# Optimization experiments

Measured on AMD Instinct MI355X. Metric: run time of the kernel, lower is better.

The kernel has to match this reference:

```python
import jax, jax.numpy as jnp
import numpy as np

N_ROLES = 6
EPS = 1e-5

def _ln(x, scale, bias):
    m = jnp.mean(x, axis=-1, keepdims=True)
    v = jnp.var(x, axis=-1, keepdims=True)
    return (x - m) * jax.lax.rsqrt(v + EPS) * scale + bias

def setup_inputs() -> dict:
    key = jax.random.key(0)
    ks = jax.random.split(key, 20)
    T, B, D_OBS, H, A = 32, 1024, 256, 512, 32
    inp = {
        'rnn_states': jax.random.normal(ks[0], (B, H), jnp.float32),
        'obs': jax.random.normal(ks[1], (T, B, D_OBS), jnp.float32),
        'resets': jnp.zeros((T, B), jnp.float32),
        'available_actions': jnp.ones((T, B, A), jnp.float32),
        'role_ids': jax.random.randint(ks[2], (T, B), 0, N_ROLES, jnp.int32),
        # feature norm over obs_dim
        'fn_scale': jnp.ones((D_OBS,), jnp.float32),
        'fn_bias': jnp.zeros((D_OBS,), jnp.float32),
        # base MLP: obs_dim->512->512, each followed by LayerNorm
        'W0': jax.random.normal(ks[3], (D_OBS, H), jnp.float32) * 0.02,
        'b0': jnp.zeros((H,), jnp.float32),
        'ln0_scale': jnp.ones((H,), jnp.float32),
        'ln0_bias': jnp.zeros((H,), jnp.float32),
        'W1': jax.random.normal(ks[4], (H, H), jnp.float32) * 0.02,
        'b1': jnp.zeros((H,), jnp.float32),
        'ln1_scale': jnp.ones((H,), jnp.float32),
        'ln1_bias': jnp.zeros((H,), jnp.float32),
        # per-role routes: obs_dim->128->H (stacked over roles)
        'Wr0': jax.random.normal(ks[5], (N_ROLES, D_OBS, 128), jnp.float32) * 0.02,
        'br0': jnp.zeros((N_ROLES, 128), jnp.float32),
        'Wr1': jax.random.normal(ks[6], (N_ROLES, 128, H), jnp.float32) * 0.02,
        'br1': jnp.zeros((N_ROLES, H), jnp.float32),
        # per-role heads: H->64->32->action_dim (stacked over roles)
        'Wh0': jax.random.normal(ks[7], (N_ROLES, H, 64), jnp.float32) * 0.02,
        'bh0': jnp.zeros((N_ROLES, 64), jnp.float32),
        'Wh1': jax.random.normal(ks[8], (N_ROLES, 64, 32), jnp.float32) * 0.02,
        'bh1': jnp.zeros((N_ROLES, 32), jnp.float32),
        'Wh2': jax.random.normal(ks[9], (N_ROLES, 32, A), jnp.float32) * 0.02,
        'bh2': jnp.zeros((N_ROLES, A), jnp.float32),
    }
    return inp

def _gather_by_role(all_values, role_ids):
    # all_values: (K, T, B, F); role_ids: (T, B) -> (T, B, F)
    idx = role_ids[None, :, :, None].astype(jnp.int32)
    return jnp.take_along_axis(all_values, idx, axis=0)[0]

def reference(rnn_states, obs, resets, available_actions, role_ids,
              fn_scale, fn_bias, W0, b0, ln0_scale, ln0_bias,
              W1, b1, ln1_scale, ln1_bias,
              Wr0, br0, Wr1, br1,
              Wh0, bh0, Wh1, bh1, Wh2, bh2):
    # feature normalization on raw obs
    obs_n = _ln(obs, fn_scale, fn_bias)
    # shared base MLP (relu + LayerNorm after each Dense)
    e = _ln(jax.nn.relu(obs_n @ W0 + b0), ln0_scale, ln0_bias)
    e = _ln(jax.nn.relu(e @ W1 + b1), ln1_scale, ln1_bias)
    # per-role pre-GRU residual routes on (normalized) obs
    r = jax.nn.relu(jnp.einsum('tbi,kih->ktbh', obs_n, Wr0) + br0[:, None, None, :])
    r = jax.nn.relu(jnp.einsum('ktbh,kho->ktbo', r, Wr1) + br1[:, None, None, :])
    e = e + _gather_by_role(r, role_ids)
    # no recurrent policy configured: rnn_states pass through
    # per-role heads -> all logits (K, T, B, A)
    h = jax.nn.relu(jnp.einsum('tbh,khf->ktbf', e, Wh0) + bh0[:, None, None, :])
    h = jax.nn.relu(jnp.einsum('ktbf,kfg->ktbg', h, Wh1) + bh1[:, None, None, :])
    all_logits = jnp.einsum('ktbg,kga->ktba', h, Wh2) + bh2[:, None, None, :]
    logits = _gather_by_role(all_logits, role_ids)
    logits = jnp.where(available_actions > 0.5, logits, jnp.full_like(logits, -1e10))
    return rnn_states, logits
```

## Files before the change

kernel.cpp:

```cpp
#include <hip/hip_runtime.h>
#include <stdint.h>

typedef unsigned short u16;
typedef unsigned int u32;

using bf16x8 = __attribute__((ext_vector_type(8))) short;
using f32x4  = __attribute__((ext_vector_type(4))) float;

#define DEVINL __device__ __forceinline__

DEVINL float b2f(u16 u) { return __builtin_bit_cast(float, (u32)u << 16); }
DEVINL u16 f2b(float f) {
  u32 u = __builtin_bit_cast(u32, f);
  u += 0x7FFFu + ((u >> 16) & 1u);
  return (u16)(u >> 16);
}

DEVINL void tp_tile(const float* __restrict__ s, u16* __restrict__ d,
                    int R, int C, int bx, int by, int z)
{
  __shared__ u16 tile[32][33];
  const size_t mstride = (size_t)R * C;
  s += (size_t)z * mstride;
  d += (size_t)z * mstride;
  int r0 = bx * 32, c0 = by * 32;
  int tx = threadIdx.x & 31, ty = threadIdx.x >> 5;
#pragma unroll
  for (int i = 0; i < 32; i += 8)
    tile[ty + i][tx] = f2b(s[(size_t)(r0 + ty + i) * C + (c0 + tx)]);
  __syncthreads();
#pragma unroll
  for (int i = 0; i < 32; i += 8)
    d[(size_t)(c0 + ty + i) * R + (r0 + tx)] = tile[tx][ty + i];
}

__global__ __launch_bounds__(256) void transpose_all(
    const float* W0, const float* W1, const float* Wr0, const float* Wr1, const float* Wh0,
    u16* W0t, u16* W1t, u16* Wr0t, u16* Wr1t, u16* Wh0t)
{
  int b = blockIdx.x;
  if (b < 128)      {            tp_tile(W0, W0t, 256, 512, b % 8,  b / 8, 0); }
  else if (b < 384) { b -= 128;  tp_tile(W1, W1t, 512, 512, b % 16, b / 16, 0); }
  else if (b < 576) { b -= 384;  int t = b / 8;  tp_tile(Wr0, Wr0t, 256, 128, b % 8,  t % 4,  t / 4); }
  else if (b < 960) { b -= 576;  int t = b / 4;  tp_tile(Wr1, Wr1t, 128, 512, b % 4,  t % 16, t / 16); }
  else              { b -= 960;  int t = b / 16; tp_tile(Wh0, Wh0t, 512, 64,  b % 16, t % 2,  t / 2); }
}

__global__ __launch_bounds__(256) void ln_f32_256(
    const float* __restrict__ X, const float* __restrict__ sc,
    const float* __restrict__ bi, u16* __restrict__ Y, int nrows)
{
  constexpr int D = 256, PER = 4;
  int lane = threadIdx.x & 63;
  int row = blockIdx.x * 4 + (threadIdx.x >> 6);
  if (row >= nrows) return;
  const float* xr = X + (size_t)row * D + lane * PER;
  float x[PER] __attribute__((aligned(16)));
  *(float4*)x = *(const float4*)xr;
  float s = 0.f, s2 = 0.f;
#pragma unroll
  for (int p = 0; p < PER; ++p) { s += x[p]; s2 += x[p] * x[p]; }
#pragma unroll
  for (int o = 32; o > 0; o >>= 1) { s += __shfl_xor(s, o, 64); s2 += __shfl_xor(s2, o, 64); }
  float m = s * (1.f / D);
  float v = s2 * (1.f / D) - m * m;
  float inv = rsqrtf(v + 1e-5f);
  u16 yu[PER] __attribute__((aligned(8)));
#pragma unroll
  for (int p = 0; p < PER; ++p)
    yu[p] = f2b((x[p] - m) * inv * sc[lane * PER + p] + bi[lane * PER + p]);
  *(uint2*)(Y + (size_t)row * D + lane * PER) = *(uint2*)yu;
}

__global__ __launch_bounds__(256) void ln_bf16_512(
    const u16* __restrict__ X, const float* __restrict__ sc,
    const float* __restrict__ bi, u16* __restrict__ Y, int nrows)
{
  constexpr int D = 512, PER = 8;
  int lane = threadIdx.x & 63;
  int row = blockIdx.x * 4 + (threadIdx.x >> 6);
  if (row >= nrows) return;
  const u16* xr = X + (size_t)row * D + lane * PER;
  u16 xu[PER] __attribute__((aligned(16)));
  *(uint4*)xu = *(const uint4*)xr;
  float x[PER]; float s = 0.f, s2 = 0.f;
#pragma unroll
  for (int p = 0; p < PER; ++p) { x[p] = b2f(xu[p]); s += x[p]; s2 += x[p] * x[p]; }
#pragma unroll
  for (int o = 32; o > 0; o >>= 1) { s += __shfl_xor(s, o, 64); s2 += __shfl_xor(s2, o, 64); }
  float m = s * (1.f / D);
  float v = s2 * (1.f / D) - m * m;
  float inv = rsqrtf(v + 1e-5f);
  u16 yu[PER] __attribute__((aligned(16)));
#pragma unroll
  for (int p = 0; p < PER; ++p)
    yu[p] = f2b((x[p] - m) * inv * sc[lane * PER + p] + bi[lane * PER + p]);
  *(uint4*)(Y + (size_t)row * D + lane * PER) = *(uint4*)yu;
}

#define NROLE 6
__global__ __launch_bounds__(256) void role_count(
    const int* __restrict__ rid, int* __restrict__ blkCnt)
{
  __shared__ int h[NROLE];
  if (threadIdx.x < NROLE) h[threadIdx.x] = 0;
  __syncthreads();
  int i = blockIdx.x * 256 + threadIdx.x;
  atomicAdd(&h[rid[i]], 1);
  __syncthreads();
  if (threadIdx.x < NROLE) blkCnt[blockIdx.x * NROLE + threadIdx.x] = h[threadIdx.x];
}

__global__ __launch_bounds__(256) void role_scan(
    const int* __restrict__ blkCnt, int* __restrict__ blkBase,
    int* __restrict__ baseArr, int* __restrict__ cntArr)
{
  __shared__ int c[128 * NROLE];
  __shared__ int bb[128 * NROLE];
  __shared__ int sbase[NROLE], scnt[NROLE];
  for (int i = threadIdx.x; i < 128 * NROLE; i += 256) c[i] = blkCnt[i];
  __syncthreads();
  if (threadIdx.x < NROLE) {
    int k = threadIdx.x, run = 0;
    for (int b = 0; b < 128; ++b) { bb[b * NROLE + k] = run; run += c[b * NROLE + k]; }
    scnt[k] = run;
  }
  __syncthreads();
  if (threadIdx.x == 0) {
    int r = 0;
    for (int k = 0; k < NROLE; ++k) { sbase[k] = r; r += scnt[k]; }
  }
  __syncthreads();
  if (threadIdx.x < NROLE) { baseArr[threadIdx.x] = sbase[threadIdx.x]; cntArr[threadIdx.x] = scnt[threadIdx.x]; }
  for (int i = threadIdx.x; i < 128 * NROLE; i += 256)
    blkBase[i] = bb[i] + sbase[i % NROLE];
}

__global__ __launch_bounds__(256) void role_fill(
    const int* __restrict__ rid, const int* __restrict__ blkBase, int* __restrict__ bucket)
{
  __shared__ int h[NROLE];
  if (threadIdx.x < NROLE) h[threadIdx.x] = 0;
  __syncthreads();
  int i = blockIdx.x * 256 + threadIdx.x;
  int k = rid[i];
  int pos = atomicAdd(&h[k], 1);
  bucket[blkBase[blockIdx.x * NROLE + k] + pos] = i;
}

enum { GM_DENSE = 0, GM_GATHER = 1, GM_CONTIG = 2, GM_GATHER_ADD = 3 };

template <int BN, int MODE>
__global__ __launch_bounds__(512, 4) void gemm_bf16(
    const u16* __restrict__ A, const u16* __restrict__ Bt,
    const float* __restrict__ bias, u16* __restrict__ C,
    const u16* __restrict__ E,
    const int* __restrict__ bucket, const int* __restrict__ baseArr,
    const int* __restrict__ cntArr, int M, int N, int K, int ldc)
{
  constexpr int BM = 256, BK = 64;
  constexpr int NF = BN / 32;
  constexpr int BR = BN / 64;
  __shared__ __align__(16) u16 As[BM * BK];
  __shared__ __align__(16) u16 Bs[BN * BK];
  const int tid = threadIdx.x;
  const int role = blockIdx.z;
  const int rowBase = blockIdx.x * BM;
  int limit;
  if constexpr (MODE == GM_DENSE) limit = M; else limit = cntArr[role];
  if (rowBase >= limit) return;
  int roleBase = 0;
  if constexpr (MODE != GM_DENSE) roleBase = baseArr[role];
  const u16* BtK = Bt + (size_t)role * N * K + (size_t)blockIdx.y * BN * K;
  const float* biasK = bias + (size_t)role * N + (size_t)blockIdx.y * BN;

  const int lane = tid & 63;
  const int wave = tid >> 6;

  const int swcol = (((tid & 7) ^ ((tid >> 3) & 7)) * 8);

  u32 aOff[4];
#pragma unroll
  for (int r = 0; r < 4; ++r) {
    int arow = r * 64 + (tid >> 3);
    int i = rowBase + arow;
    if (i >= limit) i = rowBase;
    int grow;
    if constexpr (MODE == GM_DENSE)       grow = i;
    else if constexpr (MODE == GM_GATHER) grow = bucket[roleBase + i];
    else                                  grow = roleBase + i;
    aOff[r] = (u32)grow * (u32)K + (u32)swcol;
  }
  u32 bOff[BR];
#pragma unroll
  for (int r = 0; r < BR; ++r)
    bOff[r] = (u32)(r * 64 + (tid >> 3)) * (u32)K + (u32)swcol;

  f32x4 acc[4][NF] = {};

  const int wm = (wave >> 1) * 64;
  const int wn = (wave & 1) * (NF * 16);
  const int quad = lane >> 4;
  const int lm = lane & 15;
  const int l7 = lm & 7;

  for (int k0 = 0; k0 < K; k0 += BK) {
#pragma unroll
    for (int r = 0; r < 4; ++r)
      __builtin_amdgcn_global_load_lds(
          (const __attribute__((address_space(1))) void*)(uintptr_t)(A + aOff[r] + k0),
          (__attribute__((address_space(3))) void*)(&As[r * 4096 + wave * 512]),
          16, 0, 0);
#pragma unroll
    for (int r = 0; r < BR; ++r)
      __builtin_amdgcn_global_load_lds(
          (const __attribute__((address_space(1))) void*)(uintptr_t)(BtK + bOff[r] + k0),
          (__attribute__((address_space(3))) void*)(&Bs[r * 4096 + wave * 512]),
          16, 0, 0);
    __syncthreads();
#pragma unroll
    for (int kk = 0; kk < BK; kk += 32) {
      const int kc = kk >> 3;
      bf16x8 af[4], bfr[NF];
#pragma unroll
      for (int i2 = 0; i2 < 4; ++i2) {
        int ar = wm + i2 * 16 + lm;
        af[i2] = *(const bf16x8*)&As[ar * 64 + (((quad + kc) ^ l7) * 8)];
      }
#pragma unroll
      for (int j = 0; j < NF; ++j) {
        int br = wn + j * 16 + lm;
        bfr[j] = *(const bf16x8*)&Bs[br * 64 + (((quad + kc) ^ l7) * 8)];
      }
#pragma unroll
      for (int i2 = 0; i2 < 4; ++i2)
#pragma unroll
        for (int j = 0; j < NF; ++j)
          acc[i2][j] = __builtin_amdgcn_mfma_f32_16x16x32_bf16(af[i2], bfr[j], acc[i2][j], 0, 0, 0);
    }
    __syncthreads();
  }

#pragma unroll
  for (int i2 = 0; i2 < 4; ++i2) {
#pragma unroll
    for (int r2 = 0; r2 < 4; ++r2) {
      int lrow = wm + i2 * 16 + quad * 4 + r2;
      int i = rowBase + lrow;
      if (i >= limit) continue;
      size_t crow, erow = 0;
      if constexpr (MODE == GM_DENSE) crow = (size_t)i;
      else                            crow = (size_t)(roleBase + i);
      if constexpr (MODE == GM_GATHER_ADD) erow = (size_t)bucket[roleBase + i];
#pragma unroll
      for (int j = 0; j < NF; ++j) {
        int lcol = wn + j * 16 + lm;
        float v = fmaxf(acc[i2][j][r2] + biasK[lcol], 0.f);
        size_t col = (size_t)blockIdx.y * BN + lcol;
        if constexpr (MODE == GM_GATHER_ADD) v += b2f(E[erow * (size_t)ldc + col]);
        C[crow * (size_t)ldc + col] = f2b(v);
      }
    }
  }
}

__global__ __launch_bounds__(256) void head_tail(
    const u16* __restrict__ h0buf, const int* __restrict__ bucket,
    const int* __restrict__ baseArr,
    const float* __restrict__ Wh1, const float* __restrict__ bh1,
    const float* __restrict__ Wh2, const float* __restrict__ bh2,
    const float* __restrict__ avail, float* __restrict__ outLogits)
{
  int lane = threadIdx.x & 63;
  int p = blockIdx.x * 4 + (threadIdx.x >> 6);
  int row = bucket[p];
  int k = 0;
#pragma unroll
  for (int j = 1; j < NROLE; ++j) k += (p >= baseArr[j]);
  float h0 = b2f(h0buf[(size_t)p * 64 + lane]);
  int n = lane & 31, half = lane >> 5;
  const float* W1k = Wh1 + k * 64 * 32;
  float a1 = 0.f;
#pragma unroll
  for (int jj = 0; jj < 32; ++jj) {
    int j = half * 32 + jj;
    float hj = __shfl(h0, j, 64);
    a1 += hj * W1k[j * 32 + n];
  }
  a1 += __shfl_xor(a1, 32, 64);
  float h1 = fmaxf(a1 + bh1[k * 32 + n], 0.f);
  const float* W2k = Wh2 + k * 32 * 32;
  float a2 = 0.f;
#pragma unroll
  for (int nn = 0; nn < 32; ++nn) {
    float hn = __shfl(h1, nn, 64);
    a2 += hn * W2k[nn * 32 + n];
  }
  float logit = a2 + bh2[k * 32 + n];
  float av = avail[(size_t)row * 32 + n];
  if (av <= 0.5f) logit = -1e10f;
  if (half == 0) outLogits[(size_t)row * 32 + n] = logit;
}

extern "C" void kernel_launch(void* const* d_in, const int* in_sizes, int n_in,
                              void* d_out, int out_size, void* d_ws, size_t ws_size,
                              hipStream_t stream)
{
  const float* rnn  = (const float*)d_in[0];
  const float* obs  = (const float*)d_in[1];
  const float* avail= (const float*)d_in[3];
  const int*   rid  = (const int*)d_in[4];
  const float* fn_s = (const float*)d_in[5];
  const float* fn_b = (const float*)d_in[6];
  const float* W0   = (const float*)d_in[7];
  const float* b0   = (const float*)d_in[8];
  const float* ln0s = (const float*)d_in[9];
  const float* ln0b = (const float*)d_in[10];
  const float* W1   = (const float*)d_in[11];
  const float* b1   = (const float*)d_in[12];
  const float* ln1s = (const float*)d_in[13];
  const float* ln1b = (const float*)d_in[14];
  const float* Wr0  = (const float*)d_in[15];
  const float* br0  = (const float*)d_in[16];
  const float* Wr1  = (const float*)d_in[17];
  const float* br1  = (const float*)d_in[18];
  const float* Wh0  = (const float*)d_in[19];
  const float* bh0  = (const float*)d_in[20];
  const float* Wh1  = (const float*)d_in[21];
  const float* bh1  = (const float*)d_in[22];
  const float* Wh2  = (const float*)d_in[23];
  const float* bh2  = (const float*)d_in[24];

  const int ROWS = 32768;

  char* w = (char*)d_ws;
  auto carve = [&](size_t bytes) { char* p = w; w += (bytes + 255) & ~(size_t)255; return p; };
  u16* obs_n  = (u16*)carve((size_t)ROWS * 256 * 2);
  u16* bufA   = (u16*)carve((size_t)ROWS * 512 * 2);
  u16* bufB   = (u16*)carve((size_t)ROWS * 512 * 2);
  u16* r_buf  = (u16*)carve((size_t)ROWS * 128 * 2);
  u16* h0buf  = (u16*)carve((size_t)ROWS * 64 * 2);
  u16* W0t    = (u16*)carve((size_t)512 * 256 * 2);
  u16* W1t    = (u16*)carve((size_t)512 * 512 * 2);
  u16* Wr0t   = (u16*)carve((size_t)6 * 128 * 256 * 2);
  u16* Wr1t   = (u16*)carve((size_t)6 * 512 * 128 * 2);
  u16* Wh0t   = (u16*)carve((size_t)6 * 64 * 512 * 2);
  int* bucket = (int*)carve((size_t)ROWS * 4);
  int* blkCnt = (int*)carve((size_t)128 * NROLE * 4);
  int* blkBase= (int*)carve((size_t)128 * NROLE * 4);
  int* baseArr= (int*)carve(256);
  int* cntArr = (int*)carve(256);

  float* outLogits = (float*)d_out + (size_t)1024 * 512;

  hipMemcpyAsync(d_out, rnn, (size_t)1024 * 512 * 4, hipMemcpyDeviceToDevice, stream);

  transpose_all<<<1152, 256, 0, stream>>>(W0, W1, Wr0, Wr1, Wh0, W0t, W1t, Wr0t, Wr1t, Wh0t);

  ln_f32_256<<<8192, 256, 0, stream>>>(obs, fn_s, fn_b, obs_n, ROWS);

  role_count<<<128, 256, 0, stream>>>(rid, blkCnt);
  role_scan<<<1, 256, 0, stream>>>(blkCnt, blkBase, baseArr, cntArr);
  role_fill<<<128, 256, 0, stream>>>(rid, blkBase, bucket);

  gemm_bf16<128, GM_DENSE><<<dim3(128, 4, 1), 512, 0, stream>>>(
      obs_n, W0t, b0, bufA, nullptr, nullptr, nullptr, nullptr, ROWS, 512, 256, 512);
  ln_bf16_512<<<8192, 256, 0, stream>>>(bufA, ln0s, ln0b, bufB, ROWS);
  gemm_bf16<128, GM_DENSE><<<dim3(128, 4, 1), 512, 0, stream>>>(
      bufB, W1t, b1, bufA, nullptr, nullptr, nullptr, nullptr, ROWS, 512, 512, 512);
  ln_bf16_512<<<8192, 256, 0, stream>>>(bufA, ln1s, ln1b, bufB, ROWS);

  gemm_bf16<128, GM_GATHER><<<dim3(128, 1, 6), 512, 0, stream>>>(
      obs_n, Wr0t, br0, r_buf, nullptr, bucket, baseArr, cntArr, ROWS, 128, 256, 128);
  gemm_bf16<128, GM_GATHER_ADD><<<dim3(128, 4, 6), 512, 0, stream>>>(
      r_buf, Wr1t, br1, bufA, bufB, bucket, baseArr, cntArr, ROWS, 512, 128, 512);

  gemm_bf16<64, GM_CONTIG><<<dim3(128, 1, 6), 512, 0, stream>>>(
      bufA, Wh0t, bh0, h0buf, nullptr, bucket, baseArr, cntArr, ROWS, 64, 512, 64);

  head_tail<<<8192, 256, 0, stream>>>(h0buf, bucket, baseArr, Wh1, bh1, Wh2, bh2, avail, outLogits);
}
```

Before: 302.3 us.

## Fuse LayerNorm into base GEMMs and compact role-grouped GEMM grids

Replaces the dense base-MLP GEMM plus separate LayerNorm kernels with a fused gemm_ln kernel. Each block covers a full 512-wide output row tile, so bias, ReLU and LayerNorm are applied in the epilogue using a cross-wave shared-memory reduction, removing two kernel launches and a round trip of the intermediate through memory. The per-role GEMMs are rewritten with BM=128 and BK=128, 256-thread blocks and a flattened 1D tile index that walks the role counts, so no blocks are launched empty for short roles. The trade-off is that gemm_ln reads B fragments directly from global memory without LDS staging, and its small 64-row tiles may cut reuse of the weights.

```diff
diff --git a/kernel.cpp b/kernel.cpp
--- a/kernel.cpp
+++ b/kernel.cpp
@@ -14,6 +14,12 @@
   u32 u = __builtin_bit_cast(u32, f);
   u += 0x7FFFu + ((u >> 16) & 1u);
   return (u16)(u >> 16);
+}
+
+DEVINL void gll16(const u16* src, u16* dst) {
+  __builtin_amdgcn_global_load_lds(
+      (const __attribute__((address_space(1))) void*)(uintptr_t)src,
+      (__attribute__((address_space(3))) void*)(uintptr_t)dst, 16, 0, 0);
 }
 
 DEVINL void tp_tile(const float* __restrict__ s, u16* __restrict__ d,
@@ -72,32 +78,6 @@
   *(uint2*)(Y + (size_t)row * D + lane * PER) = *(uint2*)yu;
 }
 
-__global__ __launch_bounds__(256) void ln_bf16_512(
-    const u16* __restrict__ X, const float* __restrict__ sc,
-    const float* __restrict__ bi, u16* __restrict__ Y, int nrows)
-{
-  constexpr int D = 512, PER = 8;
-  int lane = threadIdx.x & 63;
-  int row = blockIdx.x * 4 + (threadIdx.x >> 6);
-  if (row >= nrows) return;
-  const u16* xr = X + (size_t)row * D + lane * PER;
-  u16 xu[PER] __attribute__((aligned(16)));
-  *(uint4*)xu = *(const uint4*)xr;
-  float x[PER]; float s = 0.f, s2 = 0.f;
-#pragma unroll
-  for (int p = 0; p < PER; ++p) { x[p] = b2f(xu[p]); s += x[p]; s2 += x[p] * x[p]; }
-#pragma unroll
-  for (int o = 32; o > 0; o >>= 1) { s += __shfl_xor(s, o, 64); s2 += __shfl_xor(s2, o, 64); }
-  float m = s * (1.f / D);
-  float v = s2 * (1.f / D) - m * m;
-  float inv = rsqrtf(v + 1e-5f);
-  u16 yu[PER] __attribute__((aligned(16)));
-#pragma unroll
-  for (int p = 0; p < PER; ++p)
-    yu[p] = f2b((x[p] - m) * inv * sc[lane * PER + p] + bi[lane * PER + p]);
-  *(uint4*)(Y + (size_t)row * D + lane * PER) = *(uint4*)yu;
-}
-
 #define NROLE 6
 __global__ __launch_bounds__(256) void role_count(
     const int* __restrict__ rid, int* __restrict__ blkCnt)
@@ -148,90 +128,185 @@
   bucket[blkBase[blockIdx.x * NROLE + k] + pos] = i;
 }
 
-enum { GM_DENSE = 0, GM_GATHER = 1, GM_CONTIG = 2, GM_GATHER_ADD = 3 };
+template <int K>
+__global__ __launch_bounds__(256, 2) void gemm_ln(
+    const u16* __restrict__ A, const u16* __restrict__ Bt,
+    const float* __restrict__ bias, const float* __restrict__ lnsc,
+    const float* __restrict__ lnbi, u16* __restrict__ C)
+{
+  constexpr int BM = 64, BK = 64;
+  __shared__ __align__(16) u16 As[BM * BK];
+  __shared__ float redS[64][4];
+  __shared__ float redSS[64][4];
+  __shared__ float prm[1536];
+  const int tid = threadIdx.x;
+  const int rowBase = blockIdx.x * BM;
+  const int lane = tid & 63, wave = tid >> 6;
+#pragma unroll
+  for (int i = tid; i < 512; i += 256) {
+    prm[i] = bias[i]; prm[512 + i] = lnsc[i]; prm[1024 + i] = lnbi[i];
+  }
+  u32 aOff[2];
+#pragma unroll
+  for (int r = 0; r < 2; ++r) {
+    int row = r * 32 + (tid >> 3);
+    int chunk = tid & 7;
+    aOff[r] = (u32)(rowBase + row) * (u32)K + (u32)((chunk ^ (row & 7)) * 8);
+  }
+  const int quad = lane >> 4, lm = lane & 15, l7 = lm & 7;
+  const int wn = wave * 128;
+  u32 bOff[8];
+#pragma unroll
+  for (int j = 0; j < 8; ++j)
+    bOff[j] = (u32)(wn + j * 16 + lm) * (u32)K + (u32)(quad * 8);
+
+  f32x4 acc[4][8] = {};
+
+  for (int k0 = 0; k0 < K; k0 += BK) {
+#pragma unroll
+    for (int r = 0; r < 2; ++r)
+      gll16(A + aOff[r] + k0, &As[r * 2048 + wave * 512]);
+    __syncthreads();
+#pragma unroll
+    for (int kk = 0; kk < BK; kk += 32) {
+      const int kc = kk >> 3;
+      bf16x8 af[4], bfr[8];
+#pragma unroll
+      for (int i2 = 0; i2 < 4; ++i2)
+        af[i2] = *(const bf16x8*)&As[(i2 * 16 + lm) * 64 + (((quad + kc) ^ l7) * 8)];
+#pragma unroll
+      for (int j = 0; j < 8; ++j)
+        bfr[j] = *(const bf16x8*)(Bt + bOff[j] + k0 + kk);
+#pragma unroll
+      for (int i2 = 0; i2 < 4; ++i2)
+#pragma unroll
+        for (int j = 0; j < 8; ++j)
+          acc[i2][j] = __builtin_amdgcn_mfma_f32_16x16x32_bf16(af[i2], bfr[j], acc[i2][j], 0, 0, 0);
+    }
+    __syncthreads();
+  }
+
+#pragma unroll
+  for (int i2 = 0; i2 < 4; ++i2) {
+#pragma unroll
+    for (int r2 = 0; r2 < 4; ++r2) {
+      float s = 0.f, ss = 0.f;
+#pragma unroll
+      for (int j = 0; j < 8; ++j) {
+        float v = acc[i2][j][r2] + prm[wn + j * 16 + lm];
+        v = fmaxf(v, 0.f);
+        acc[i2][j][r2] = v;
+        s += v; ss += v * v;
+      }
+#pragma unroll
+      for (int o = 1; o < 16; o <<= 1) { s += __shfl_xor(s, o, 64); ss += __shfl_xor(ss, o, 64); }
+      if (lm == 0) {
+        int rowL = i2 * 16 + quad * 4 + r2;
+        redS[rowL][wave] = s;
+        redSS[rowL][wave] = ss;
+      }
+    }
+  }
+  __syncthreads();
+#pragma unroll
+  for (int i2 = 0; i2 < 4; ++i2) {
+#pragma unroll
+    for (int r2 = 0; r2 < 4; ++r2) {
+      int rowL = i2 * 16 + quad * 4 + r2;
+      float ts  = redS[rowL][0] + redS[rowL][1] + redS[rowL][2] + redS[rowL][3];
+      float tss = redSS[rowL][0] + redSS[rowL][1] + redSS[rowL][2] + redSS[rowL][3];
+      float m = ts * (1.f / 512.f);
+      float var = tss * (1.f / 512.f) - m * m;
+      float inv = rsqrtf(var + 1e-5f);
+      size_t base = (size_t)(rowBase + rowL) * 512;
+#pragma unroll
+      for (int j = 0; j < 8; ++j) {
+        int col = wn + j * 16 + lm;
+        float y = (acc[i2][j][r2] - m) * inv * prm[512 + col] + prm[1024 + col];
+        C[base + col] = f2b(y);
+      }
+    }
+  }
+}
+
+enum { GM_GATHER = 1, GM_CONTIG = 2, GM_GATHER_ADD = 3 };
 
 template <int BN, int MODE>
-__global__ __launch_bounds__(512, 4) void gemm_bf16(
+__global__ __launch_bounds__(256, 2) void gemm_bk128(
     const u16* __restrict__ A, const u16* __restrict__ Bt,
     const float* __restrict__ bias, u16* __restrict__ C,
     const u16* __restrict__ E,
     const int* __restrict__ bucket, const int* __restrict__ baseArr,
-    const int* __restrict__ cntArr, int M, int N, int K, int ldc)
-{
-  constexpr int BM = 256, BK = 64;
+    const int* __restrict__ cntArr, int K, int ldc)
+{
+  constexpr int BM = 128, BK = 128;
   constexpr int NF = BN / 32;
-  constexpr int BR = BN / 64;
+  constexpr int AR = BM * BK / 2048;
+  constexpr int BR2 = BN * BK / 2048;
   __shared__ __align__(16) u16 As[BM * BK];
   __shared__ __align__(16) u16 Bs[BN * BK];
   const int tid = threadIdx.x;
-  const int role = blockIdx.z;
-  const int rowBase = blockIdx.x * BM;
-  int limit;
-  if constexpr (MODE == GM_DENSE) limit = M; else limit = cntArr[role];
-  if (rowBase >= limit) return;
-  int roleBase = 0;
-  if constexpr (MODE != GM_DENSE) roleBase = baseArr[role];
+
+  int role = 0, rem = blockIdx.x, cnt;
+  for (;;) {
+    cnt = cntArr[role];
+    int tiles = (cnt + BM - 1) >> 7;
+    if (rem < tiles) break;
+    rem -= tiles;
+    if (++role >= NROLE) return;
+  }
+  const int limit = cnt;
+  const int rowBase = rem * BM;
+  const int roleBase = baseArr[role];
+  const int N = gridDim.y * BN;
   const u16* BtK = Bt + (size_t)role * N * K + (size_t)blockIdx.y * BN * K;
   const float* biasK = bias + (size_t)role * N + (size_t)blockIdx.y * BN;
 
-  const int lane = tid & 63;
-  const int wave = tid >> 6;
-
-  const int swcol = (((tid & 7) ^ ((tid >> 3) & 7)) * 8);
-
-  u32 aOff[4];
-#pragma unroll
-  for (int r = 0; r < 4; ++r) {
-    int arow = r * 64 + (tid >> 3);
-    int i = rowBase + arow;
+  const int lane = tid & 63, wave = tid >> 6;
+
+  u32 aOff[AR];
+#pragma unroll
+  for (int r = 0; r < AR; ++r) {
+    int row = r * 16 + (tid >> 4);
+    int chunk = tid & 15;
+    int i = rowBase + row;
     if (i >= limit) i = rowBase;
     int grow;
-    if constexpr (MODE == GM_DENSE)       grow = i;
-    else if constexpr (MODE == GM_GATHER) grow = bucket[roleBase + i];
-    else                                  grow = roleBase + i;
-    aOff[r] = (u32)grow * (u32)K + (u32)swcol;
-  }
-  u32 bOff[BR];
-#pragma unroll
-  for (int r = 0; r < BR; ++r)
-    bOff[r] = (u32)(r * 64 + (tid >> 3)) * (u32)K + (u32)swcol;
+    if constexpr (MODE == GM_GATHER) grow = bucket[roleBase + i];
+    else                             grow = roleBase + i;
+    aOff[r] = (u32)grow * (u32)K + (u32)((chunk ^ (row & 7)) * 8);
+  }
+  u32 bOff[BR2];
+#pragma unroll
+  for (int r = 0; r < BR2; ++r) {
+    int brow = r * 16 + (tid >> 4);
+    int chunk = tid & 15;
+    bOff[r] = (u32)brow * (u32)K + (u32)((chunk ^ (brow & 7)) * 8);
+  }
 
   f32x4 acc[4][NF] = {};
-
   const int wm = (wave >> 1) * 64;
   const int wn = (wave & 1) * (NF * 16);
-  const int quad = lane >> 4;
-  const int lm = lane & 15;
-  const int l7 = lm & 7;
+  const int quad = lane >> 4, lm = lane & 15, l7 = lm & 7;
 
   for (int k0 = 0; k0 < K; k0 += BK) {
 #pragma unroll
-    for (int r = 0; r < 4; ++r)
-      __builtin_amdgcn_global_load_lds(
-          (const __attribute__((address_space(1))) void*)(uintptr_t)(A + aOff[r] + k0),
-          (__attribute__((address_space(3))) void*)(&As[r * 4096 + wave * 512]),
-          16, 0, 0);
-#pragma unroll
-    for (int r = 0; r < BR; ++r)
-      __builtin_amdgcn_global_load_lds(
-          (const __attribute__((address_space(1))) void*)(uintptr_t)(BtK + bOff[r] + k0),
-          (__attribute__((address_space(3))) void*)(&Bs[r * 4096 + wave * 512]),
-          16, 0, 0);
+    for (int r = 0; r < AR; ++r)
+      gll16(A + aOff[r] + k0, &As[r * 2048 + wave * 512]);
+#pragma unroll
+    for (int r = 0; r < BR2; ++r)
+      gll16(BtK + bOff[r] + k0, &Bs[r * 2048 + wave * 512]);
     __syncthreads();
 #pragma unroll
     for (int kk = 0; kk < BK; kk += 32) {
       const int kc = kk >> 3;
       bf16x8 af[4], bfr[NF];
 #pragma unroll
-      for (int i2 = 0; i2 < 4; ++i2) {
-        int ar = wm + i2 * 16 + lm;
-        af[i2] = *(const bf16x8*)&As[ar * 64 + (((quad + kc) ^ l7) * 8)];
-      }
-#pragma unroll
-      for (int j = 0; j < NF; ++j) {
-        int br = wn + j * 16 + lm;
-        bfr[j] = *(const bf16x8*)&Bs[br * 64 + (((quad + kc) ^ l7) * 8)];
-      }
+      for (int i2 = 0; i2 < 4; ++i2)
+        af[i2] = *(const bf16x8*)&As[(wm + i2 * 16 + lm) * 128 + (((quad + kc) ^ l7) * 8)];
+#pragma unroll
+      for (int j = 0; j < NF; ++j)
+        bfr[j] = *(const bf16x8*)&Bs[(wn + j * 16 + lm) * 128 + (((quad + kc) ^ l7) * 8)];
 #pragma unroll
       for (int i2 = 0; i2 < 4; ++i2)
 #pragma unroll
@@ -248,9 +323,7 @@
       int lrow = wm + i2 * 16 + quad * 4 + r2;
       int i = rowBase + lrow;
       if (i >= limit) continue;
-      size_t crow, erow = 0;
-      if constexpr (MODE == GM_DENSE) crow = (size_t)i;
-      else                            crow = (size_t)(roleBase + i);
+      size_t crow = (size_t)(roleBase + i), erow = 0;
       if constexpr (MODE == GM_GATHER_ADD) erow = (size_t)bucket[roleBase + i];
 #pragma unroll
       for (int j = 0; j < NF; ++j) {
@@ -363,20 +436,16 @@
   role_scan<<<1, 256, 0, stream>>>(blkCnt, blkBase, baseArr, cntArr);
   role_fill<<<128, 256, 0, stream>>>(rid, blkBase, bucket);
 
-  gemm_bf16<128, GM_DENSE><<<dim3(128, 4, 1), 512, 0, stream>>>(
-      obs_n, W0t, b0, bufA, nullptr, nullptr, nullptr, nullptr, ROWS, 512, 256, 512);
-  ln_bf16_512<<<8192, 256, 0, stream>>>(bufA, ln0s, ln0b, bufB, ROWS);
-  gemm_bf16<128, GM_DENSE><<<dim3(128, 4, 1), 512, 0, stream>>>(
-      bufB, W1t, b1, bufA, nullptr, nullptr, nullptr, nullptr, ROWS, 512, 512, 512);
-  ln_bf16_512<<<8192, 256, 0, stream>>>(bufA, ln1s, ln1b, bufB, ROWS);
-
-  gemm_bf16<128, GM_GATHER><<<dim3(128, 1, 6), 512, 0, stream>>>(
-      obs_n, Wr0t, br0, r_buf, nullptr, bucket, baseArr, cntArr, ROWS, 128, 256, 128);
-  gemm_bf16<128, GM_GATHER_ADD><<<dim3(128, 4, 6), 512, 0, stream>>>(
-      r_buf, Wr1t, br1, bufA, bufB, bucket, baseArr, cntArr, ROWS, 512, 128, 512);
-
-  gemm_bf16<64, GM_CONTIG><<<dim3(128, 1, 6), 512, 0, stream>>>(
-      bufA, Wh0t, bh0, h0buf, nullptr, bucket, baseArr, cntArr, ROWS, 64, 512, 64);
+  gemm_ln<256><<<512, 256, 0, stream>>>(obs_n, W0t, b0, ln0s, ln0b, bufA);
+  gemm_ln<512><<<512, 256, 0, stream>>>(bufA, W1t, b1, ln1s, ln1b, bufB);
+
+  gemm_bk128<128, GM_GATHER><<<dim3(261, 1), 256, 0, stream>>>(
+      obs_n, Wr0t, br0, r_buf, nullptr, bucket, baseArr, cntArr, 256, 128);
+  gemm_bk128<128, GM_GATHER_ADD><<<dim3(261, 4), 256, 0, stream>>>(
+      r_buf, Wr1t, br1, bufA, bufB, bucket, baseArr, cntArr, 128, 512);
+
+  gemm_bk128<64, GM_CONTIG><<<dim3(261, 1), 256, 0, stream>>>(
+      bufA, Wh0t, bh0, h0buf, nullptr, bucket, baseArr, cntArr, 512, 64);
 
   head_tail<<<8192, 256, 0, stream>>>(h0buf, bucket, baseArr, Wh1, bh1, Wh2, bh2, avail, outLogits);
 }
```

Result: slower. 310.3 us (+2.6%).
